# Performance work log

Hardware: AMD Instinct MI355X
Metric: run time of the kernel (lower is better)

Reference implementation:

```python
import jax, jax.numpy as jnp
import numpy as np

HIDDEN = 4544
NUM_HEADS = 71
HEAD_DIM = 64
ROPE_BASE = 10000.0


def _rope_cos_sin(seq_len, dim, dtype):
    inv_freq = 1.0 / (ROPE_BASE ** (jnp.arange(0, dim, 2, dtype=jnp.float32) / dim))
    t = jnp.arange(seq_len, dtype=jnp.float32)
    freqs = jnp.einsum('i,j->ij', t, inv_freq)            # [S, dim/2]
    emb = jnp.concatenate([freqs, freqs], axis=-1)        # [S, dim]
    return jnp.cos(emb).astype(dtype), jnp.sin(emb).astype(dtype)


def _rotate_half(x):
    half = x.shape[-1] // 2
    return jnp.concatenate([-x[..., half:], x[..., :half]], axis=-1)


def _apply_rope(x, cos, sin):
    # x: [..., S, hd]; cos/sin: [S, hd]
    return x * cos + _rotate_half(x) * sin


def setup_inputs() -> dict:
    key = jax.random.key(0)
    k1, k2, k3 = jax.random.split(key, 3)
    B, S = 1, 1024
    hidden_states = jax.random.normal(k1, (B, 1, S, HIDDEN), dtype=jnp.float32) * 0.02
    # additive causal mask (prefill)
    neg = jnp.triu(jnp.full((S, S), -1e9, dtype=jnp.float32), k=1)
    attention_mask = jnp.broadcast_to(neg[None, None], (B, 1, S, S))
    # fused QKV weight (already transposed for right-matmul): [H, (nh+2)*hd]
    qkv_w = jax.random.normal(k2, (HIDDEN, (NUM_HEADS + 2) * HEAD_DIM), dtype=jnp.float32) * 0.02
    dense_w = jax.random.normal(k3, (HIDDEN, HIDDEN), dtype=jnp.float32) * 0.02
    return {"hidden_states": hidden_states, "attention_mask": attention_mask,
            "qkv_w": qkv_w, "dense_w": dense_w}


def reference(hidden_states, attention_mask, qkv_w, dense_w):
    B, _, S, H = hidden_states.shape
    nh, hd = NUM_HEADS, HEAD_DIM
    x = hidden_states[:, 0]                               # [B, S, H]
    fused = jnp.einsum('bsh,hf->bsf', x, qkv_w)           # [B, S, (nh+2)*hd]
    fused = fused.reshape(B, S, nh + 2, hd)
    q = jnp.transpose(fused[:, :, :nh, :], (0, 2, 1, 3))  # [B, nh, S, hd]
    k = fused[:, :, nh, :]                                # [B, S, hd]  (single KV head, MQA)
    v = fused[:, :, nh + 1, :]                            # [B, S, hd]
    cos, sin = _rope_cos_sin(S, hd, q.dtype)
    q = _apply_rope(q, cos, sin)
    k = _apply_rope(k, cos, sin)
    scale = 1.0 / np.sqrt(hd).astype(np.float32)
    scores = jnp.einsum('bhsd,btd->bhst', q, k) * scale   # [B, nh, S, S]
    scores = scores + attention_mask                      # broadcast over heads
    probs = jax.nn.softmax(scores, axis=-1)
    ctx = jnp.einsum('bhst,btd->bhsd', probs, v)          # [B, nh, S, hd]
    ctx = jnp.transpose(ctx, (0, 2, 1, 3)).reshape(B, S, nh * hd)
    out = jnp.einsum('bsh,hg->bsg', ctx, dense_w)         # [B, S, H]
    return out[:, None]                                   # [B, 1, S, H]
```

## Files before the change

kernel.cpp:

```cpp
#include <hip/hip_runtime.h>

#define S_LEN 1024
#define HID   4544
#define NH    71
#define NQKV  4672
#define NQKV_PAD 4736
#define ND_PAD   4608

#define XB (S_LEN * HID / 1024)
#define WB ((NQKV_PAD / 64) * (HID / 64))
#define RB 128

typedef __attribute__((ext_vector_type(4)))  float f32x4;
typedef __attribute__((ext_vector_type(4))) unsigned short u16x4;
typedef __attribute__((ext_vector_type(8))) unsigned short u16x8;
typedef __attribute__((ext_vector_type(8))) __bf16 bf16x8;

__device__ __forceinline__ bf16x8 as_bf(u16x8 v) { return __builtin_bit_cast(bf16x8, v); }

__device__ __forceinline__ unsigned short f2bf(float f) {
    unsigned u = __builtin_bit_cast(unsigned, f);
    return (unsigned short)((u + 0x7FFFu + ((u >> 16) & 1u)) >> 16);
}
__device__ __forceinline__ float bf2f(unsigned short u) {
    return __builtin_bit_cast(float, (unsigned)u << 16);
}
__device__ __forceinline__ unsigned pk2(float a, float b) {
    return (unsigned)f2bf(a) | ((unsigned)f2bf(b) << 16);
}
__device__ __forceinline__ void gload16(const void* g, void* l) {
    __builtin_amdgcn_global_load_lds((const __attribute__((address_space(1))) unsigned int*)g,
                                     (__attribute__((address_space(3))) unsigned int*)l,
                                     16, 0, 0);
}

__global__ __launch_bounds__(256) void prep_kernel(
        const float4* __restrict__ x, ushort4* __restrict__ y,
        const float* __restrict__ qkv_w, unsigned short* __restrict__ wqkvT,
        float* __restrict__ cs, float* __restrict__ sn) {
    __shared__ float tb[64][65];
    int bx = blockIdx.x, t = threadIdx.x;
    if (bx < XB) {
        int i = bx * 256 + t;
        float4 v = x[i];
        ushort4 r;
        r.x = f2bf(v.x); r.y = f2bf(v.y); r.z = f2bf(v.z); r.w = f2bf(v.w);
        y[i] = r;
    } else if (bx < XB + WB) {
        int idx = bx - XB;
        int n0 = (idx % (NQKV_PAD / 64)) * 64, k0 = (idx / (NQKV_PAD / 64)) * 64;
        int tx = t & 15, ty = t >> 4;
#pragma unroll
        for (int r = 0; r < 64; r += 16) {
            int k = k0 + ty + r, n = n0 + tx * 4;
            float4 v = make_float4(0.f, 0.f, 0.f, 0.f);
            if (n < NQKV) v = *(const float4*)&qkv_w[(size_t)k * NQKV + n];
            tb[ty + r][tx * 4 + 0] = v.x;
            tb[ty + r][tx * 4 + 1] = v.y;
            tb[ty + r][tx * 4 + 2] = v.z;
            tb[ty + r][tx * 4 + 3] = v.w;
        }
        __syncthreads();
        int nr = t >> 2, kq = (t & 3) * 16;
        unsigned short tmp[16];
#pragma unroll
        for (int z = 0; z < 16; z++) tmp[z] = f2bf(tb[kq + z][nr]);
        u16x8* dst = (u16x8*)&wqkvT[(size_t)(n0 + nr) * HID + k0 + kq];
        dst[0] = *(const u16x8*)&tmp[0];
        dst[1] = *(const u16x8*)&tmp[8];
    } else {
        int gi = (bx - XB - WB) * 256 + t;
        int s = gi >> 5, i = gi & 31;
        float inv = powf(10000.0f, -(2.0f * (float)i) / 64.0f);
        float f = (float)s * inv;
        cs[s * 32 + i] = cosf(f);
        sn[s * 32 + i] = sinf(f);
    }
}

template<int EPI>
__global__ __launch_bounds__(128, 2) void gemm_bt_kernel(
        const unsigned short* __restrict__ A, const unsigned short* __restrict__ BT,
        void* __restrict__ Cout, const float* __restrict__ cs_t,
        const float* __restrict__ sn_t, unsigned short* __restrict__ k_out,
        unsigned short* __restrict__ v_out, int K, int ldc, int n_store,
        const float* __restrict__ w2, unsigned short* __restrict__ wt2,
        int gemm_blocks) {
    __shared__ char smem[49152];
    unsigned short* As0 = (unsigned short*)smem;
    unsigned short* Bs0 = (unsigned short*)(smem + 16384);
    int t = threadIdx.x;

    if ((int)blockIdx.x >= gemm_blocks) {
        float (*tb)[65] = (float(*)[65])smem;
        int idx = (int)blockIdx.x - gemm_blocks;
        int n0 = (idx % (ND_PAD / 64)) * 64, k0 = (idx / (ND_PAD / 64)) * 64;
        int tx = t & 15, ty = t >> 4;
#pragma unroll
        for (int r = 0; r < 64; r += 8) {
            int k = k0 + ty + r, n = n0 + tx * 4;
            float4 v = make_float4(0.f, 0.f, 0.f, 0.f);
            if (n < HID) v = *(const float4*)&w2[(size_t)k * HID + n];
            tb[ty + r][tx * 4 + 0] = v.x;
            tb[ty + r][tx * 4 + 1] = v.y;
            tb[ty + r][tx * 4 + 2] = v.z;
            tb[ty + r][tx * 4 + 3] = v.w;
        }
        __syncthreads();
        int nr = t >> 1, kh = (t & 1) * 32;
        unsigned short tmp[32];
#pragma unroll
        for (int z = 0; z < 32; z++) tmp[z] = f2bf(tb[kh + z][nr]);
        u16x8* dst = (u16x8*)&wt2[(size_t)(n0 + nr) * HID + k0 + kh];
        dst[0] = *(const u16x8*)&tmp[0];
        dst[1] = *(const u16x8*)&tmp[8];
        dst[2] = *(const u16x8*)&tmp[16];
        dst[3] = *(const u16x8*)&tmp[24];
        return;
    }

    int p = blockIdx.x;
    int per = gemm_blocks >> 3;
    int l = (p & 7) * per + (p >> 3);
    int msl = l & 15, nb = l >> 4;
    int m0 = msl * 64, n0 = nb * 128;
    int wn = t >> 6;
    int lane = t & 63, lr = lane & 15, lg = lane >> 4;

    f32x4 acc[4][4];
#pragma unroll
    for (int mi = 0; mi < 4; mi++)
#pragma unroll
        for (int ni = 0; ni < 4; ni++) acc[mi][ni] = (f32x4)0.0f;

    const char* Ab = (const char*)A;
    const char* Bb = (const char*)BT;
    size_t rs = (size_t)K * 2;

    auto stage = [&](int step, int buf) {
        size_t kb = (size_t)step * 128;
#pragma unroll
        for (int i = 0; i < 4; i++) {
            int chunk = i * 128 + t;
            int row = chunk >> 3, c8 = chunk & 7;
            int csrc = c8 ^ (row & 7);
            gload16(Ab + (size_t)(m0 + row) * rs + kb + csrc * 16,
                    (char*)As0 + buf * 8192 + chunk * 16);
        }
#pragma unroll
        for (int i = 0; i < 8; i++) {
            int chunk = i * 128 + t;
            int row = chunk >> 3, c8 = chunk & 7;
            int csrc = c8 ^ (row & 7);
            gload16(Bb + (size_t)(n0 + row) * rs + kb + csrc * 16,
                    (char*)Bs0 + buf * 16384 + chunk * 16);
        }
    };

    int nsteps = K >> 6;
    stage(0, 0);
    if (nsteps > 1) stage(1, 1);
    for (int s = 0; s < nsteps; ++s) {
        int cur = s & 1;
        if (s + 1 < nsteps) { asm volatile("s_waitcnt vmcnt(12)" ::: "memory"); }
        else                { asm volatile("s_waitcnt vmcnt(0)" ::: "memory"); }
        __builtin_amdgcn_s_barrier();
        bf16x8 af[4][2], bfr[4][2];
#pragma unroll
        for (int mi = 0; mi < 4; mi++) {
            int row = mi * 16 + lr;
#pragma unroll
            for (int kk = 0; kk < 2; kk++)
                af[mi][kk] = as_bf(*(const u16x8*)&As0[cur * 4096 + row * 64 + (((kk * 4 + lg) ^ (row & 7)) << 3)]);
        }
#pragma unroll
        for (int ni = 0; ni < 4; ni++) {
            int row = wn * 64 + ni * 16 + lr;
#pragma unroll
            for (int kk = 0; kk < 2; kk++)
                bfr[ni][kk] = as_bf(*(const u16x8*)&Bs0[cur * 8192 + row * 64 + (((kk * 4 + lg) ^ (row & 7)) << 3)]);
        }
        asm volatile("s_waitcnt lgkmcnt(0)" ::: "memory");
        __builtin_amdgcn_s_barrier();
        if (s + 2 < nsteps) stage(s + 2, cur);
#pragma unroll
        for (int kk = 0; kk < 2; kk++)
#pragma unroll
            for (int mi = 0; mi < 4; mi++)
#pragma unroll
                for (int ni = 0; ni < 4; ni++)
                    acc[mi][ni] = __builtin_amdgcn_mfma_f32_16x16x32_bf16(
                        af[mi][kk], bfr[ni][kk], acc[mi][ni], 0, 0, 0);
    }

    if (EPI == 0) {
        float* C = (float*)Cout;
#pragma unroll
        for (int mi = 0; mi < 4; mi++)
#pragma unroll
            for (int ni = 0; ni < 4; ni++) {
                int col = n0 + wn * 64 + ni * 16 + lr;
                if (col < n_store) {
#pragma unroll
                    for (int i = 0; i < 4; i++) {
                        int row = m0 + mi * 16 + 4 * lg + i;
                        C[(size_t)row * ldc + col] = acc[mi][ni][i];
                    }
                }
            }
    } else {
        int hh = nb * 2 + wn;
        if (hh == 72) {
#pragma unroll
            for (int mi = 0; mi < 4; mi++)
#pragma unroll
                for (int ni = 0; ni < 4; ni++) {
                    int d = ni * 16 + lr;
                    int s0 = m0 + mi * 16 + 4 * lg;
                    u16x4 pk;
#pragma unroll
                    for (int i = 0; i < 4; i++) pk[i] = f2bf(acc[mi][ni][i]);
                    *(u16x4*)&v_out[(size_t)d * S_LEN + s0] = pk;
                }
        } else if (hh < 72) {
            unsigned short* qb = (unsigned short*)Cout;
            float qscale = (hh < 71) ? 0.125f : 1.0f;
#pragma unroll
            for (int mi = 0; mi < 4; mi++)
#pragma unroll
                for (int i = 0; i < 4; i++) {
                    int s = m0 + mi * 16 + 4 * lg + i;
                    float c0 = cs_t[s * 32 + lr],      g0 = sn_t[s * 32 + lr];
                    float c1 = cs_t[s * 32 + 16 + lr], g1 = sn_t[s * 32 + 16 + lr];
#pragma unroll
                    for (int ni = 0; ni < 4; ni++) {
                        float x  = acc[mi][ni][i];
                        float xp = acc[mi][ni ^ 2][i];
                        float c = (ni & 1) ? c1 : c0;
                        float g = (ni & 1) ? g1 : g0;
                        float r = (ni < 2) ? (x * c - xp * g) : (x * c + xp * g);
                        r *= qscale;
                        int d = ni * 16 + lr;
                        if (hh < 71) qb[(size_t)s * HID + hh * 64 + d] = f2bf(r);
                        else         k_out[(size_t)s * 64 + d] = f2bf(r);
                    }
                }
        }
    }
}

__global__ __launch_bounds__(256, 3) void attn_kernel(
        const unsigned short* __restrict__ qb, const unsigned short* __restrict__ kr,
        const unsigned short* __restrict__ vt, unsigned short* __restrict__ ctx,
        unsigned short* __restrict__ Opart, float2* __restrict__ MLpart) {
    __shared__ unsigned short Ks[2][64 * 64];
    __shared__ unsigned short Vs[2][64 * 64];
    __shared__ unsigned short Pl[4][16 * 72];
    int h = blockIdx.y;
    int u = blockIdx.x;
    int c, j0;
    if (u < 16)      { c = 0; j0 = u * 4; }
    else if (u < 28) { c = 1; j0 = 16 + (u - 16) * 4; }
    else if (u < 36) { c = 2; j0 = 32 + (u - 28) * 4; }
    else             { c = 3; j0 = 48 + (u - 36) * 4; }
    int t = threadIdx.x, wv = t >> 6, lane = t & 63, lr = lane & 15, lg = lane >> 4;
    int j = j0 + wv;
    int qs = j * 16 + lr;
    int k_lo = c * 256;
    int kend_w   = min((j + 1) * 16, k_lo + 256);
    int kend_max = min((j0 + 4) * 16, k_lo + 256);
    int nt = (kend_max - k_lo) >> 6;
    int nch = (j >> 4) + 1;
    int srow = t >> 3, sc16 = t & 7, sw = lr & 7;

    auto stage = [&](int ti, int buf) {
        size_t kbase = (size_t)(k_lo + ti * 64);
#pragma unroll
        for (int i = 0; i < 2; i++) {
            int row = i * 32 + srow;
            int csrc = sc16 ^ (row & 7);
            gload16((const char*)kr + (kbase + row) * 128 + csrc * 16,
                    (char*)Ks[buf] + (i * 256 + t) * 16);
        }
#pragma unroll
        for (int i = 0; i < 2; i++) {
            int row = i * 32 + srow;
            int csrc = sc16 ^ (row & 7);
            gload16((const char*)vt + (size_t)row * 2048 + kbase * 2 + csrc * 16,
                    (char*)Vs[buf] + (i * 256 + t) * 16);
        }
    };

    bf16x8 qf[2];
#pragma unroll
    for (int dc = 0; dc < 2; dc++)
        qf[dc] = as_bf(*(const u16x8*)&qb[(size_t)qs * HID + h * 64 + dc * 32 + 8 * lg]);

    float m_i = -1e30f, l_i = 0.0f;
    f32x4 o[4];
#pragma unroll
    for (int d4 = 0; d4 < 4; d4++) o[d4] = (f32x4)0.0f;

    stage(0, 0);
    if (nt > 1) stage(1, 1);

    for (int ti = 0; ti < nt; ti++) {
        int cur = ti & 1;
        if (ti + 1 < nt) { asm volatile("s_waitcnt vmcnt(4)" ::: "memory"); }
        else             { asm volatile("s_waitcnt vmcnt(0)" ::: "memory"); }
        __builtin_amdgcn_s_barrier();
        int k0 = k_lo + ti * 64;
        if (k0 < kend_w) {
            f32x4 st[4];
#pragma unroll
            for (int nc = 0; nc < 4; nc++) st[nc] = (f32x4)0.0f;
#pragma unroll
            for (int nc = 0; nc < 4; nc++) {
                int krow = nc * 16 + lr;
#pragma unroll
                for (int dc = 0; dc < 2; dc++) {
                    bf16x8 kf = as_bf(*(const u16x8*)&Ks[cur][krow * 64 + (((dc * 4 + lg) ^ sw) << 3)]);
                    st[nc] = __builtin_amdgcn_mfma_f32_16x16x32_bf16(kf, qf[dc], st[nc], 0, 0, 0);
                }
            }
            bool needmask = (k0 + 64 > j * 16);
            float mx = -1e30f;
            if (needmask) {
#pragma unroll
                for (int nc = 0; nc < 4; nc++)
#pragma unroll
                    for (int i = 0; i < 4; i++) {
                        int ks = k0 + nc * 16 + 4 * lg + i;
                        float v = (ks <= qs) ? st[nc][i] : -1e30f;
                        st[nc][i] = v;
                        mx = fmaxf(mx, v);
                    }
            } else {
#pragma unroll
                for (int nc = 0; nc < 4; nc++)
#pragma unroll
                    for (int i = 0; i < 4; i++) mx = fmaxf(mx, st[nc][i]);
            }
            mx = fmaxf(mx, __shfl_xor(mx, 16));
            mx = fmaxf(mx, __shfl_xor(mx, 32));
            if (!__all(mx <= m_i + 8.0f)) {
                float mn = fmaxf(m_i, mx);
                float so = __expf(m_i - mn);
                l_i *= so;
#pragma unroll
                for (int d4 = 0; d4 < 4; d4++)
#pragma unroll
                    for (int i = 0; i < 4; i++) o[d4][i] *= so;
                m_i = mn;
            }
            float ps = 0.0f;
#pragma unroll
            for (int nc = 0; nc < 4; nc++)
#pragma unroll
                for (int i = 0; i < 4; i++) {
                    float v = st[nc][i];
                    float e = (!needmask || v > -1e29f) ? __expf(v - m_i) : 0.0f;
                    st[nc][i] = e;
                    ps += e;
                }
            ps += __shfl_xor(ps, 16);
            ps += __shfl_xor(ps, 32);
            l_i += ps;
#pragma unroll
            for (int nc = 0; nc < 4; nc++) {
                *(unsigned*)&Pl[wv][lr * 72 + nc * 16 + 4 * lg]     = pk2(st[nc][0], st[nc][1]);
                *(unsigned*)&Pl[wv][lr * 72 + nc * 16 + 4 * lg + 2] = pk2(st[nc][2], st[nc][3]);
            }
            bf16x8 pb[2];
#pragma unroll
            for (int kk = 0; kk < 2; kk++)
                pb[kk] = as_bf(*(const u16x8*)&Pl[wv][lr * 72 + kk * 32 + 8 * lg]);
#pragma unroll
            for (int d4 = 0; d4 < 4; d4++) {
                int vrow = d4 * 16 + lr;
#pragma unroll
                for (int kk = 0; kk < 2; kk++) {
                    bf16x8 vf = as_bf(*(const u16x8*)&Vs[cur][vrow * 64 + (((kk * 4 + lg) ^ sw) << 3)]);
                    o[d4] = __builtin_amdgcn_mfma_f32_16x16x32_bf16(vf, pb[kk], o[d4], 0, 0, 0);
                }
            }
        }
        __builtin_amdgcn_s_barrier();
        if (ti + 2 < nt) stage(ti + 2, cur);
    }

    if (nch == 1) {
        float linv = 1.0f / l_i;
#pragma unroll
        for (int d4 = 0; d4 < 4; d4++) {
            u16x4 pk;
#pragma unroll
            for (int i = 0; i < 4; i++) pk[i] = f2bf(o[d4][i] * linv);
            *(u16x4*)&ctx[(size_t)qs * HID + h * 64 + d4 * 16 + 4 * lg] = pk;
        }
    } else {
        int pi = (h * 48 + (j - 16)) * 4 + c;
#pragma unroll
        for (int d4 = 0; d4 < 4; d4++) {
            u16x4 pk;
#pragma unroll
            for (int i = 0; i < 4; i++) pk[i] = f2bf(o[d4][i]);
            *(u16x4*)&Opart[(size_t)pi * 1024 + lr * 64 + d4 * 16 + 4 * lg] = pk;
        }
        if (lg == 0) MLpart[pi * 16 + lr] = make_float2(m_i, l_i);
    }
}

__global__ __launch_bounds__(256) void merge_kernel(
        const unsigned short* __restrict__ Opart, const float2* __restrict__ MLpart,
        unsigned short* __restrict__ ctx) {
    int mu = blockIdx.x * 4 + (threadIdx.x >> 6);
    int lane = threadIdx.x & 63;
    int h = mu / 48, jj = mu % 48, j = 16 + jj;
    int nch = (j >> 4) + 1;
    int base = (h * 48 + jj) * 4;
    for (int q = 0; q < 16; q++) {
        float m[4], l[4], w[4];
        float M = -1e30f;
        for (int c = 0; c < nch; c++) {
            float2 ml = MLpart[(base + c) * 16 + q];
            m[c] = ml.x; l[c] = ml.y;
            M = fmaxf(M, m[c]);
        }
        float L = 0.0f;
        for (int c = 0; c < nch; c++) { w[c] = __expf(m[c] - M); L += l[c] * w[c]; }
        float acc = 0.0f;
        for (int c = 0; c < nch; c++)
            acc += w[c] * bf2f(Opart[(size_t)(base + c) * 1024 + q * 64 + lane]);
        ctx[(size_t)(j * 16 + q) * HID + h * 64 + lane] = f2bf(acc / L);
    }
}

extern "C" void kernel_launch(void* const* d_in, const int* in_sizes, int n_in,
                              void* d_out, int out_size, void* d_ws, size_t ws_size,
                              hipStream_t stream) {
    const float* hs      = (const float*)d_in[0];
    const float* qkv_w   = (const float*)d_in[2];
    const float* dense_w = (const float*)d_in[3];
    float* out = (float*)d_out;

    char* ws = (char*)d_ws;
    size_t off = 0;
    auto alloc = [&](size_t bytes) -> void* {
        void* p = ws + off;
        off += (bytes + 255) & ~(size_t)255;
        return p;
    };
    unsigned short* x_bf   = (unsigned short*)alloc((size_t)S_LEN * HID * 2);
    unsigned short* wqkvT  = (unsigned short*)alloc((size_t)NQKV_PAD * HID * 2);
    unsigned short* q_bf   = (unsigned short*)alloc((size_t)S_LEN * HID * 2);
    unsigned short* k_rope = (unsigned short*)alloc((size_t)S_LEN * 64 * 2);
    unsigned short* v_t    = (unsigned short*)alloc((size_t)64 * S_LEN * 2);
    unsigned short* ctx    = (unsigned short*)alloc((size_t)S_LEN * HID * 2);
    unsigned short* wdT    = (unsigned short*)alloc((size_t)ND_PAD * HID * 2);
    float*          cs_t   = (float*)alloc((size_t)S_LEN * 32 * 4);
    float*          sn_t   = (float*)alloc((size_t)S_LEN * 32 * 4);
    (void)ws_size;
    unsigned short* Opart  = wqkvT;
    float2*         MLpart = (float2*)((char*)wqkvT + (size_t)71 * 48 * 4 * 1024 * 2);

    prep_kernel<<<dim3(XB + WB + RB), dim3(256), 0, stream>>>(
        (const float4*)hs, (ushort4*)x_bf, qkv_w, wqkvT, cs_t, sn_t);

    gemm_bt_kernel<1><<<dim3(592 + (ND_PAD / 64) * (HID / 64)), dim3(128), 0, stream>>>(
        x_bf, wqkvT, q_bf, cs_t, sn_t, k_rope, v_t, HID, HID, NQKV,
        dense_w, wdT, 592);

    attn_kernel<<<dim3(40, NH), dim3(256), 0, stream>>>(
        q_bf, k_rope, v_t, ctx, Opart, MLpart);

    merge_kernel<<<dim3(NH * 48 / 4), dim3(256), 0, stream>>>(Opart, MLpart, ctx);

    gemm_bt_kernel<0><<<dim3(576), dim3(128), 0, stream>>>(
        ctx, wdT, out, nullptr, nullptr, nullptr, nullptr, HID, HID, HID,
        nullptr, nullptr, 576);
}
```

Baseline: 251.9 us.

## Move dense weight transpose from QKV GEMM launch into attention launch

The fp32-to-bf16 transpose of the dense projection weight was run as extra blocks appended to the QKV GEMM grid; it now runs as extra blocks (72 per head row) in the attention grid. The GEMM kernel goes back to a plain static shared-memory layout sized for GEMM only, and the attention kernel switches to a shared byte buffer so the transpose tile can reuse it. The aim is to overlap the memory-bound weight conversion with the attention kernel's compute-bound tail rather than with the GEMM, at the risk of adding blocks that compete with attention for CUs and lowering its occupancy.

```diff
diff --git a/kernel.cpp b/kernel.cpp
--- a/kernel.cpp
+++ b/kernel.cpp
@@ -83,47 +83,15 @@
         const unsigned short* __restrict__ A, const unsigned short* __restrict__ BT,
         void* __restrict__ Cout, const float* __restrict__ cs_t,
         const float* __restrict__ sn_t, unsigned short* __restrict__ k_out,
-        unsigned short* __restrict__ v_out, int K, int ldc, int n_store,
-        const float* __restrict__ w2, unsigned short* __restrict__ wt2,
-        int gemm_blocks) {
-    __shared__ char smem[49152];
-    unsigned short* As0 = (unsigned short*)smem;
-    unsigned short* Bs0 = (unsigned short*)(smem + 16384);
-    int t = threadIdx.x;
-
-    if ((int)blockIdx.x >= gemm_blocks) {
-        float (*tb)[65] = (float(*)[65])smem;
-        int idx = (int)blockIdx.x - gemm_blocks;
-        int n0 = (idx % (ND_PAD / 64)) * 64, k0 = (idx / (ND_PAD / 64)) * 64;
-        int tx = t & 15, ty = t >> 4;
-#pragma unroll
-        for (int r = 0; r < 64; r += 8) {
-            int k = k0 + ty + r, n = n0 + tx * 4;
-            float4 v = make_float4(0.f, 0.f, 0.f, 0.f);
-            if (n < HID) v = *(const float4*)&w2[(size_t)k * HID + n];
-            tb[ty + r][tx * 4 + 0] = v.x;
-            tb[ty + r][tx * 4 + 1] = v.y;
-            tb[ty + r][tx * 4 + 2] = v.z;
-            tb[ty + r][tx * 4 + 3] = v.w;
-        }
-        __syncthreads();
-        int nr = t >> 1, kh = (t & 1) * 32;
-        unsigned short tmp[32];
-#pragma unroll
-        for (int z = 0; z < 32; z++) tmp[z] = f2bf(tb[kh + z][nr]);
-        u16x8* dst = (u16x8*)&wt2[(size_t)(n0 + nr) * HID + k0 + kh];
-        dst[0] = *(const u16x8*)&tmp[0];
-        dst[1] = *(const u16x8*)&tmp[8];
-        dst[2] = *(const u16x8*)&tmp[16];
-        dst[3] = *(const u16x8*)&tmp[24];
-        return;
-    }
-
+        unsigned short* __restrict__ v_out, int K, int ldc, int n_store) {
+    __shared__ unsigned short As[2][64 * 64];
+    __shared__ unsigned short Bs[2][128 * 64];
     int p = blockIdx.x;
-    int per = gemm_blocks >> 3;
+    int per = gridDim.x >> 3;
     int l = (p & 7) * per + (p >> 3);
     int msl = l & 15, nb = l >> 4;
     int m0 = msl * 64, n0 = nb * 128;
+    int t = threadIdx.x;
     int wn = t >> 6;
     int lane = t & 63, lr = lane & 15, lg = lane >> 4;
 
@@ -145,7 +113,7 @@
             int row = chunk >> 3, c8 = chunk & 7;
             int csrc = c8 ^ (row & 7);
             gload16(Ab + (size_t)(m0 + row) * rs + kb + csrc * 16,
-                    (char*)As0 + buf * 8192 + chunk * 16);
+                    (char*)As[buf] + chunk * 16);
         }
 #pragma unroll
         for (int i = 0; i < 8; i++) {
@@ -153,7 +121,7 @@
             int row = chunk >> 3, c8 = chunk & 7;
             int csrc = c8 ^ (row & 7);
             gload16(Bb + (size_t)(n0 + row) * rs + kb + csrc * 16,
-                    (char*)Bs0 + buf * 16384 + chunk * 16);
+                    (char*)Bs[buf] + chunk * 16);
         }
     };
 
@@ -171,14 +139,14 @@
             int row = mi * 16 + lr;
 #pragma unroll
             for (int kk = 0; kk < 2; kk++)
-                af[mi][kk] = as_bf(*(const u16x8*)&As0[cur * 4096 + row * 64 + (((kk * 4 + lg) ^ (row & 7)) << 3)]);
+                af[mi][kk] = as_bf(*(const u16x8*)&As[cur][row * 64 + (((kk * 4 + lg) ^ (row & 7)) << 3)]);
         }
 #pragma unroll
         for (int ni = 0; ni < 4; ni++) {
             int row = wn * 64 + ni * 16 + lr;
 #pragma unroll
             for (int kk = 0; kk < 2; kk++)
-                bfr[ni][kk] = as_bf(*(const u16x8*)&Bs0[cur * 8192 + row * 64 + (((kk * 4 + lg) ^ (row & 7)) << 3)]);
+                bfr[ni][kk] = as_bf(*(const u16x8*)&Bs[cur][row * 64 + (((kk * 4 + lg) ^ (row & 7)) << 3)]);
         }
         asm volatile("s_waitcnt lgkmcnt(0)" ::: "memory");
         __builtin_amdgcn_s_barrier();
@@ -252,18 +220,48 @@
 __global__ __launch_bounds__(256, 3) void attn_kernel(
         const unsigned short* __restrict__ qb, const unsigned short* __restrict__ kr,
         const unsigned short* __restrict__ vt, unsigned short* __restrict__ ctx,
-        unsigned short* __restrict__ Opart, float2* __restrict__ MLpart) {
-    __shared__ unsigned short Ks[2][64 * 64];
-    __shared__ unsigned short Vs[2][64 * 64];
-    __shared__ unsigned short Pl[4][16 * 72];
+        unsigned short* __restrict__ Opart, float2* __restrict__ MLpart,
+        const float* __restrict__ w2, unsigned short* __restrict__ wt2) {
+    __shared__ char smem[41984];
+    unsigned short* Ks = (unsigned short*)smem;
+    unsigned short* Vs = (unsigned short*)(smem + 16384);
+    unsigned short* Pl = (unsigned short*)(smem + 32768);
     int h = blockIdx.y;
     int u = blockIdx.x;
+    int t = threadIdx.x;
+
+    if (u >= 40) {
+        float (*tb)[65] = (float(*)[65])smem;
+        int idx = (u - 40) + 72 * h;
+        int n0 = (idx % 72) * 64, k0 = (idx / 72) * 64;
+        int tx = t & 15, ty = t >> 4;
+#pragma unroll
+        for (int r = 0; r < 64; r += 16) {
+            int k = k0 + ty + r, n = n0 + tx * 4;
+            float4 v = make_float4(0.f, 0.f, 0.f, 0.f);
+            if (n < HID) v = *(const float4*)&w2[(size_t)k * HID + n];
+            tb[ty + r][tx * 4 + 0] = v.x;
+            tb[ty + r][tx * 4 + 1] = v.y;
+            tb[ty + r][tx * 4 + 2] = v.z;
+            tb[ty + r][tx * 4 + 3] = v.w;
+        }
+        __syncthreads();
+        int nr = t >> 2, kq = (t & 3) * 16;
+        unsigned short tmp[16];
+#pragma unroll
+        for (int z = 0; z < 16; z++) tmp[z] = f2bf(tb[kq + z][nr]);
+        u16x8* dst = (u16x8*)&wt2[(size_t)(n0 + nr) * HID + k0 + kq];
+        dst[0] = *(const u16x8*)&tmp[0];
+        dst[1] = *(const u16x8*)&tmp[8];
+        return;
+    }
+
     int c, j0;
     if (u < 16)      { c = 0; j0 = u * 4; }
     else if (u < 28) { c = 1; j0 = 16 + (u - 16) * 4; }
     else if (u < 36) { c = 2; j0 = 32 + (u - 28) * 4; }
     else             { c = 3; j0 = 48 + (u - 36) * 4; }
-    int t = threadIdx.x, wv = t >> 6, lane = t & 63, lr = lane & 15, lg = lane >> 4;
+    int wv = t >> 6, lane = t & 63, lr = lane & 15, lg = lane >> 4;
     int j = j0 + wv;
     int qs = j * 16 + lr;
     int k_lo = c * 256;
@@ -280,14 +278,14 @@
             int row = i * 32 + srow;
             int csrc = sc16 ^ (row & 7);
             gload16((const char*)kr + (kbase + row) * 128 + csrc * 16,
-                    (char*)Ks[buf] + (i * 256 + t) * 16);
+                    (char*)Ks + buf * 8192 + (i * 256 + t) * 16);
         }
 #pragma unroll
         for (int i = 0; i < 2; i++) {
             int row = i * 32 + srow;
             int csrc = sc16 ^ (row & 7);
             gload16((const char*)vt + (size_t)row * 2048 + kbase * 2 + csrc * 16,
-                    (char*)Vs[buf] + (i * 256 + t) * 16);
+                    (char*)Vs + buf * 8192 + (i * 256 + t) * 16);
         }
     };
 
@@ -319,7 +317,7 @@
                 int krow = nc * 16 + lr;
 #pragma unroll
                 for (int dc = 0; dc < 2; dc++) {
-                    bf16x8 kf = as_bf(*(const u16x8*)&Ks[cur][krow * 64 + (((dc * 4 + lg) ^ sw) << 3)]);
+                    bf16x8 kf = as_bf(*(const u16x8*)&Ks[cur * 4096 + krow * 64 + (((dc * 4 + lg) ^ sw) << 3)]);
                     st[nc] = __builtin_amdgcn_mfma_f32_16x16x32_bf16(kf, qf[dc], st[nc], 0, 0, 0);
                 }
             }
@@ -368,19 +366,19 @@
             l_i += ps;
 #pragma unroll
             for (int nc = 0; nc < 4; nc++) {
-                *(unsigned*)&Pl[wv][lr * 72 + nc * 16 + 4 * lg]     = pk2(st[nc][0], st[nc][1]);
-                *(unsigned*)&Pl[wv][lr * 72 + nc * 16 + 4 * lg + 2] = pk2(st[nc][2], st[nc][3]);
+                *(unsigned*)&Pl[wv * 1152 + lr * 72 + nc * 16 + 4 * lg]     = pk2(st[nc][0], st[nc][1]);
+                *(unsigned*)&Pl[wv * 1152 + lr * 72 + nc * 16 + 4 * lg + 2] = pk2(st[nc][2], st[nc][3]);
             }
             bf16x8 pb[2];
 #pragma unroll
             for (int kk = 0; kk < 2; kk++)
-                pb[kk] = as_bf(*(const u16x8*)&Pl[wv][lr * 72 + kk * 32 + 8 * lg]);
+                pb[kk] = as_bf(*(const u16x8*)&Pl[wv * 1152 + lr * 72 + kk * 32 + 8 * lg]);
 #pragma unroll
             for (int d4 = 0; d4 < 4; d4++) {
                 int vrow = d4 * 16 + lr;
 #pragma unroll
                 for (int kk = 0; kk < 2; kk++) {
-                    bf16x8 vf = as_bf(*(const u16x8*)&Vs[cur][vrow * 64 + (((kk * 4 + lg) ^ sw) << 3)]);
+                    bf16x8 vf = as_bf(*(const u16x8*)&Vs[cur * 4096 + vrow * 64 + (((kk * 4 + lg) ^ sw) << 3)]);
                     o[d4] = __builtin_amdgcn_mfma_f32_16x16x32_bf16(vf, pb[kk], o[d4], 0, 0, 0);
                 }
             }
@@ -467,16 +465,14 @@
     prep_kernel<<<dim3(XB + WB + RB), dim3(256), 0, stream>>>(
         (const float4*)hs, (ushort4*)x_bf, qkv_w, wqkvT, cs_t, sn_t);
 
-    gemm_bt_kernel<1><<<dim3(592 + (ND_PAD / 64) * (HID / 64)), dim3(128), 0, stream>>>(
-        x_bf, wqkvT, q_bf, cs_t, sn_t, k_rope, v_t, HID, HID, NQKV,
-        dense_w, wdT, 592);
-
-    attn_kernel<<<dim3(40, NH), dim3(256), 0, stream>>>(
-        q_bf, k_rope, v_t, ctx, Opart, MLpart);
+    gemm_bt_kernel<1><<<dim3(16 * NQKV_PAD / 128), dim3(128), 0, stream>>>(
+        x_bf, wqkvT, q_bf, cs_t, sn_t, k_rope, v_t, HID, HID, NQKV);
+
+    attn_kernel<<<dim3(40 + 72, NH), dim3(256), 0, stream>>>(
+        q_bf, k_rope, v_t, ctx, Opart, MLpart, dense_w, wdT);
 
     merge_kernel<<<dim3(NH * 48 / 4), dim3(256), 0, stream>>>(Opart, MLpart, ctx);
 
-    gemm_bt_kernel<0><<<dim3(576), dim3(128), 0, stream>>>(
-        ctx, wdT, out, nullptr, nullptr, nullptr, nullptr, HID, HID, HID,
-        nullptr, nullptr, 576);
-}
+    gemm_bt_kernel<0><<<dim3(16 * ND_PAD / 128), dim3(128), 0, stream>>>(
+        ctx, wdT, out, nullptr, nullptr, nullptr, nullptr, HID, HID, HID);
+}
```

Result: no change. 251.7 us (-0.1%).
